# Performance work log

Measured on AMD Instinct MI355X. Metric: run time of the kernel, lower is better.

The kernel has to match this reference:

```python
import jax, jax.numpy as jnp
import numpy as np


def _conv1x1(x, W, b):
    # x: [b,c,h,w], W: [out,in], b: [out]
    return jnp.einsum('oi,bihw->bohw', W, x) + b[None, :, None, None]


def setup_inputs() -> dict:
    key = jax.random.key(0)
    ks = jax.random.split(key, 8)
    B, C, H, W = 4, 256, 64, 64
    s = 1.0 / np.sqrt(C)
    return {
        'x1': jax.random.normal(ks[0], (B, C, H, W), jnp.float32),
        'x2': jax.random.normal(ks[1], (B, C, H, W), jnp.float32),
        'Wq': jax.random.normal(ks[2], (C, C), jnp.float32) * s,
        'bq': jax.random.normal(ks[3], (C,), jnp.float32) * 0.01,
        'Wk': jax.random.normal(ks[4], (C, C), jnp.float32) * s,
        'bk': jax.random.normal(ks[5], (C,), jnp.float32) * 0.01,
        'Wv': jax.random.normal(ks[6], (C, C), jnp.float32) * s,
        'bv': jax.random.normal(ks[7], (C,), jnp.float32) * 0.01,
    }


def reference(x1, x2, Wq, bq, Wk, bk, Wv, bv):
    b, c, h, w = x1.shape
    n = h * w
    q = _conv1x1(x1, Wq, bq).reshape(b, c, n)   # [b,c,n]
    k = _conv1x1(x2, Wk, bk).reshape(b, c, n)   # [b,c,n]
    v = _conv1x1(x2, Wv, bv).reshape(b, c, n)   # [b,c,n]
    # scores[b,i,j] = sum_c q[b,c,i] * k[b,c,j]; softmax over j (last dim)
    scores = jnp.einsum('bci,bcj->bij', q, k)
    attn = jax.nn.softmax(scores, axis=-1)      # [b,n,n]
    # out[b,c,i] = sum_j v[b,c,j] * attn[b,i,j]  (v @ attn^T)
    out = jnp.einsum('bcj,bij->bci', v, attn)
    return out.reshape(b, c, h, w)
```

## Files before the change

### kernel.cpp

```cpp
#include <hip/hip_runtime.h>

#define BATCH 4
#define CDIM 256
#define NDIM 4096
#define SPLITS 4
#define KSPLIT (NDIM / SPLITS)
#define JT 32
#define NTILES (KSPLIT / JT)

typedef unsigned short u16;
typedef unsigned int u32;
typedef _Float16 f16;
typedef __attribute__((ext_vector_type(8))) _Float16 half8;
typedef __attribute__((ext_vector_type(4))) float floatx4;

__device__ __forceinline__ void load_lds_128(const void* g, void* l) {
  __builtin_amdgcn_global_load_lds(
      (const __attribute__((address_space(1))) u32*)g,
      (__attribute__((address_space(3))) u32*)l, 16, 0, 0);
}

__global__ __launch_bounds__(256) void prep_w_k(
    const float* __restrict__ wq, const float* __restrict__ wk,
    const float* __restrict__ wv, f16* __restrict__ whq,
    f16* __restrict__ whk, f16* __restrict__ whv) {
  const int gid = blockIdx.x * 256 + threadIdx.x;
  const int a = gid >> 13;
  const int r = gid & 8191;
  const float* src = (a == 0) ? wq : ((a == 1) ? wk : wv);
  f16* dst = (a == 0) ? whq : ((a == 1) ? whk : whv);
  float4 v0 = *(const float4*)(src + r * 8);
  float4 v1 = *(const float4*)(src + r * 8 + 4);
  half8 h;
  h[0] = (f16)v0.x; h[1] = (f16)v0.y; h[2] = (f16)v0.z; h[3] = (f16)v0.w;
  h[4] = (f16)v1.x; h[5] = (f16)v1.y; h[6] = (f16)v1.z; h[7] = (f16)v1.w;
  *(half8*)(dst + r * 8) = h;
}

__global__ __launch_bounds__(512, 2) void proj_fused_k(
    const float* __restrict__ x1, const float* __restrict__ x2,
    const f16* __restrict__ whq, const float* __restrict__ bq,
    const f16* __restrict__ whk, const float* __restrict__ bk,
    const f16* __restrict__ whv, const float* __restrict__ bv,
    f16* __restrict__ qt, f16* __restrict__ kt, f16* __restrict__ vsp) {
  __shared__ __align__(16) u16 xtt[128 * 264];
  const int j0 = blockIdx.x * 128;
  const int b = blockIdx.y;
  const int z = blockIdx.z;
  const float* xs = ((z == 0) ? x1 : x2) + (size_t)b * CDIM * NDIM;
  const int t = threadIdx.x;
  const int wave = t >> 6, lane = t & 63, l16 = lane & 15, grp = lane >> 4;

#pragma unroll
  for (int it = 0; it < 16; ++it) {
    const int task = wave + it * 8;
    const int c4 = task >> 1;
    const int n = (task & 1) * 64 + lane;
    const float* gp = xs + (size_t)(c4 * 4) * NDIM + j0 + n;
    float v0 = gp[0];
    float v1 = gp[NDIM];
    float v2 = gp[2 * NDIM];
    float v3 = gp[3 * NDIM];
    union { f16 h[4]; uint2 u; } pk;
    pk.h[0] = (f16)v0; pk.h[1] = (f16)v1; pk.h[2] = (f16)v2; pk.h[3] = (f16)v3;
    *(uint2*)&xtt[n * 264 + c4 * 4] = pk.u;
  }
  __syncthreads();
  const f16* xth = (const f16*)xtt;

  {
    const f16* w = (z == 0) ? whq : whk;
    const float* bias = (z == 0) ? bq : bk;
    f16* outp = ((z == 0) ? qt : kt) + (size_t)b * NDIM * CDIM;
    const int jb0 = (wave & 3) * 32;
    const int cw = (wave >> 2) * 128;
    floatx4 acc[2][8];
#pragma unroll
    for (int mb = 0; mb < 2; ++mb)
#pragma unroll
      for (int nb = 0; nb < 8; ++nb) acc[mb][nb] = (floatx4){0.f, 0.f, 0.f, 0.f};
#pragma unroll
    for (int ks = 0; ks < 8; ++ks) {
      half8 a[2];
#pragma unroll
      for (int mb = 0; mb < 2; ++mb) {
        const int n = jb0 + mb * 16 + l16;
        a[mb] = *(const half8*)&xth[n * 264 + ks * 32 + grp * 8];
      }
      __builtin_amdgcn_s_setprio(1);
#pragma unroll
      for (int nb = 0; nb < 8; ++nb) {
        half8 bb = *(const half8*)(w + (size_t)(cw + nb * 16 + l16) * CDIM + ks * 32 + grp * 8);
        acc[0][nb] = __builtin_amdgcn_mfma_f32_16x16x32_f16(a[0], bb, acc[0][nb], 0, 0, 0);
        acc[1][nb] = __builtin_amdgcn_mfma_f32_16x16x32_f16(a[1], bb, acc[1][nb], 0, 0, 0);
      }
      __builtin_amdgcn_s_setprio(0);
    }
#pragma unroll
    for (int nb = 0; nb < 8; ++nb) {
      const int c = cw + nb * 16 + l16;
      const float bvv = bias[c];
#pragma unroll
      for (int mb = 0; mb < 2; ++mb) {
        const int jbase = j0 + jb0 + mb * 16 + grp * 4;
#pragma unroll
        for (int r = 0; r < 4; ++r)
          outp[(size_t)(jbase + r) * CDIM + c] = (f16)(acc[mb][nb][r] + bvv);
      }
    }
  }

  if (z == 1) {
    f16* outp = vsp + (size_t)b * CDIM * NDIM;
    const int cw = (wave & 1) * 128;
    const int jw = (wave >> 1) * 32;
    floatx4 acc[8][2];
#pragma unroll
    for (int mb = 0; mb < 8; ++mb)
#pragma unroll
      for (int nb = 0; nb < 2; ++nb) acc[mb][nb] = (floatx4){0.f, 0.f, 0.f, 0.f};
#pragma unroll
    for (int ks = 0; ks < 8; ++ks) {
      half8 a[8];
#pragma unroll
      for (int mb = 0; mb < 8; ++mb)
        a[mb] = *(const half8*)(whv + (size_t)(cw + mb * 16 + l16) * CDIM + ks * 32 + grp * 8);
#pragma unroll
      for (int nb = 0; nb < 2; ++nb) {
        const int n = jw + nb * 16 + l16;
        half8 bv8 = *(const half8*)&xth[n * 264 + ks * 32 + grp * 8];
        __builtin_amdgcn_s_setprio(1);
#pragma unroll
        for (int mb = 0; mb < 8; ++mb)
          acc[mb][nb] = __builtin_amdgcn_mfma_f32_16x16x32_f16(a[mb], bv8, acc[mb][nb], 0, 0, 0);
        __builtin_amdgcn_s_setprio(0);
      }
    }
#pragma unroll
    for (int mb = 0; mb < 8; ++mb)
#pragma unroll
      for (int r = 0; r < 4; ++r) {
        const int c = cw + mb * 16 + grp * 4 + r;
        const float bvv = bv[c];
#pragma unroll
        for (int nb = 0; nb < 2; ++nb) {
          const int j = j0 + jw + nb * 16 + l16;
          outp[(size_t)c * NDIM + j] = (f16)(acc[mb][nb][r] + bvv);
        }
      }
  }
}

__global__ __launch_bounds__(512, 4) void flash_k(
    const f16* __restrict__ qt, const f16* __restrict__ kt,
    const f16* __restrict__ vs, f16* __restrict__ pO,
    float* __restrict__ pm, float* __restrict__ pl) {
  __shared__ __align__(16) u16 smem[32768 + 5120];
  const int bx = blockIdx.x;
  const int c16 = bx & 15;
  const int b = c16 >> 2, s = c16 & 3;
  const int i0 = (bx >> 4) * 128;
  const int jwin = s * KSPLIT;
  const f16* Q = qt + (size_t)b * NDIM * CDIM;
  const f16* K = kt + (size_t)b * NDIM * CDIM;
  const f16* V = vs + (size_t)b * CDIM * NDIM;
  const int tid = threadIdx.x;
  const int wave = tid >> 6, lane = tid & 63, l16 = lane & 15, grp = lane >> 4;
  f16* Pw = (f16*)(smem + 32768) + wave * (16 * 40);

  half8 qf[8];
#pragma unroll
  for (int ks = 0; ks < 8; ++ks)
    qf[ks] = *(const half8*)(Q + (size_t)(i0 + wave * 16 + l16) * CDIM + ks * 32 + grp * 8);

  floatx4 O[16];
#pragma unroll
  for (int cb = 0; cb < 16; ++cb) O[cb] = (floatx4){0.f, 0.f, 0.f, 0.f};
  float m_ = -1e30f;
  float lsum = 0.f;

  const int kr2 = lane >> 5, kp = lane & 31;
  const int vrow = lane >> 2, vp = lane & 3;

#define STAGE(J0, BUF)                                                         \
  {                                                                            \
    u16* sK = smem + (BUF) * 16384;                                            \
    u16* sV = sK + 8192;                                                       \
    _Pragma("unroll") for (int it = 0; it < 2; ++it) {                         \
      const int row = wave * 4 + it * 2 + kr2;                                 \
      const int g = kp ^ (row & 7);                                            \
      load_lds_128(K + (size_t)((J0) + row) * CDIM + g * 8,                    \
                   &sK[(wave * 4 + it * 2) * 256]);                            \
    }                                                                          \
    _Pragma("unroll") for (int it = 0; it < 2; ++it) {                         \
      const int c = wave * 32 + it * 16 + vrow;                                \
      const int g = vp ^ ((c >> 2) & 3);                                       \
      load_lds_128(V + (size_t)c * NDIM + (J0) + g * 8,                        \
                   &sV[(wave * 32 + it * 16) * 32]);                           \
    }                                                                          \
  }

  STAGE(jwin, 0)

  for (int tt = 0; tt < NTILES; ++tt) {
    __syncthreads();
    if (tt + 1 < NTILES) STAGE(jwin + (tt + 1) * JT, (tt + 1) & 1)
    u16* bK = smem + (tt & 1) * 16384;
    u16* bV = bK + 8192;

    floatx4 S[2];
#pragma unroll
    for (int jb = 0; jb < 2; ++jb) S[jb] = (floatx4){0.f, 0.f, 0.f, 0.f};
    __builtin_amdgcn_s_setprio(1);
#pragma unroll
    for (int ks = 0; ks < 8; ++ks) {
      const int chunk = ks * 4 + grp;
#pragma unroll
      for (int jb = 0; jb < 2; ++jb) {
        const int row = jb * 16 + l16;
        half8 kf = *(const half8*)&bK[row * 256 + ((chunk ^ (row & 7)) << 3)];
        S[jb] = __builtin_amdgcn_mfma_f32_16x16x32_f16(qf[ks], kf, S[jb], 0, 0, 0);
      }
    }
    __builtin_amdgcn_s_setprio(0);

#pragma unroll
    for (int jb = 0; jb < 2; ++jb)
#pragma unroll
      for (int r = 0; r < 4; ++r)
        Pw[(grp * 4 + r) * 40 + jb * 16 + l16] = (f16)S[jb][r];
    half8 rawh = *(const half8*)&Pw[l16 * 40 + grp * 8];
    float u[8];
#pragma unroll
    for (int j = 0; j < 8; ++j) u[j] = (float)rawh[j];
    float mx = fmaxf(fmaxf(fmaxf(u[0], u[1]), fmaxf(u[2], u[3])),
                     fmaxf(fmaxf(u[4], u[5]), fmaxf(u[6], u[7])));
    mx = fmaxf(mx, __shfl_xor(mx, 16, 64));
    mx = fmaxf(mx, __shfl_xor(mx, 32, 64));
    const float mnew = fmaxf(m_, mx);
    const float alpha = __expf(m_ - mnew);
    m_ = mnew;
    float pe[8];
#pragma unroll
    for (int j = 0; j < 8; ++j) pe[j] = __expf(u[j] - mnew);
    const float ps = ((pe[0] + pe[1]) + (pe[2] + pe[3])) +
                     ((pe[4] + pe[5]) + (pe[6] + pe[7]));
    lsum = lsum * alpha + ps;
    half8 pa;
#pragma unroll
    for (int j = 0; j < 8; ++j) pa[j] = (f16)pe[j];

    if (__any(alpha < 1.f)) {
#pragma unroll
      for (int cb = 0; cb < 16; ++cb) O[cb] *= alpha;
    }

    __builtin_amdgcn_s_setprio(1);
#pragma unroll
    for (int cb = 0; cb < 16; ++cb) {
      const int c = cb * 16 + l16;
      half8 vf = *(const half8*)&bV[c * 32 + ((grp ^ ((c >> 2) & 3)) << 3)];
      O[cb] = __builtin_amdgcn_mfma_f32_16x16x32_f16(vf, pa, O[cb], 0, 0, 0);
    }
    __builtin_amdgcn_s_setprio(0);
  }

  lsum += __shfl_xor(lsum, 16, 64);
  lsum += __shfl_xor(lsum, 32, 64);
  if (grp == 0) {
    const int base = (b * SPLITS + s) * NDIM + i0;
    const int i = wave * 16 + l16;
    pm[base + i] = m_;
    pl[base + i] = lsum;
  }

  const size_t pbase = (size_t)(b * SPLITS + s) * CDIM * NDIM;
  const int i = i0 + wave * 16 + l16;
#pragma unroll
  for (int cb = 0; cb < 16; ++cb) {
    const int c = cb * 16 + grp * 4;
#pragma unroll
    for (int r = 0; r < 4; ++r)
      pO[pbase + (size_t)(c + r) * NDIM + i] = (f16)O[cb][r];
  }
}

__global__ __launch_bounds__(256) void combine_k(
    const f16* __restrict__ pO, const float* __restrict__ pm,
    const float* __restrict__ pl, float* __restrict__ out) {
  __shared__ float su[SPLITS][64];
  const int b = blockIdx.x >> 6;
  const int i0 = (blockIdx.x & 63) * 64;
  const int t = threadIdx.x;
  if (t < 64) {
    const int i = i0 + t;
    float mv[SPLITS], w[SPLITS];
    float M = -3e38f;
#pragma unroll
    for (int s = 0; s < SPLITS; ++s) {
      mv[s] = pm[(b * SPLITS + s) * NDIM + i];
      M = fmaxf(M, mv[s]);
    }
    float L = 0.f;
#pragma unroll
    for (int s = 0; s < SPLITS; ++s) {
      w[s] = __expf(mv[s] - M);
      L += pl[(b * SPLITS + s) * NDIM + i] * w[s];
    }
    const float invL = 1.0f / L;
#pragma unroll
    for (int s = 0; s < SPLITS; ++s) su[s][t] = w[s] * invL;
  }
  __syncthreads();
#pragma unroll
  for (int it = 0; it < 8; ++it) {
    const int task = t + it * 256;
    const int c = task >> 3, p = (task & 7) * 8;
    float acc[8] = {0.f, 0.f, 0.f, 0.f, 0.f, 0.f, 0.f, 0.f};
#pragma unroll
    for (int s = 0; s < SPLITS; ++s) {
      const f16* src = pO + ((size_t)(b * SPLITS + s) * CDIM + c) * NDIM + i0 + p;
      half8 h = *(const half8*)src;
#pragma unroll
      for (int j = 0; j < 8; ++j) acc[j] += su[s][p + j] * (float)h[j];
    }
    float* dst = out + ((size_t)b * CDIM + c) * NDIM + i0 + p;
    float4 lo = {acc[0], acc[1], acc[2], acc[3]};
    float4 hi = {acc[4], acc[5], acc[6], acc[7]};
    *(float4*)dst = lo;
    *(float4*)(dst + 4) = hi;
  }
}

extern "C" void kernel_launch(void* const* d_in, const int* in_sizes, int n_in,
                              void* d_out, int out_size, void* d_ws, size_t ws_size,
                              hipStream_t stream) {
  const float* x1 = (const float*)d_in[0];
  const float* x2 = (const float*)d_in[1];
  const float* Wq = (const float*)d_in[2];
  const float* bq = (const float*)d_in[3];
  const float* Wk = (const float*)d_in[4];
  const float* bk = (const float*)d_in[5];
  const float* Wv = (const float*)d_in[6];
  const float* bv = (const float*)d_in[7];
  float* out = (float*)d_out;
  char* ws = (char*)d_ws;
  f16* qtp = (f16*)(ws + 0);
  f16* ktp = (f16*)(ws + 8388608);
  f16* vsp = (f16*)(ws + 16777216);
  f16* pO = (f16*)(ws + 25165824);
  float* pm = (float*)(ws + 58720256);
  float* pl = (float*)(ws + 58982400);
  f16* whq = (f16*)(ws + 41943040);
  f16* whk = whq + CDIM * CDIM;
  f16* whv = whk + CDIM * CDIM;

  prep_w_k<<<dim3(96), dim3(256), 0, stream>>>(Wq, Wk, Wv, whq, whk, whv);
  proj_fused_k<<<dim3(NDIM / 128, BATCH, 2), dim3(512), 0, stream>>>(
      x1, x2, whq, bq, whk, bk, whv, bv, qtp, ktp, vsp);
  flash_k<<<dim3(512), dim3(512), 0, stream>>>(qtp, ktp, vsp, pO, pm, pl);
  combine_k<<<dim3(256), dim3(256), 0, stream>>>(pO, pm, pl, out);
}
```

Before: 249.3 us.

## Single-buffer flash LDS and add 8-way KV split when workspace allows

The flash kernel drops LDS double buffering, loading each K/V tile into a single buffer with a sync before and after compute. This halves shared memory per block so more blocks can be resident. When the workspace is large enough it also uses 8 KV splits with 1024 blocks instead of 4 splits and 512 blocks, which doubles parallelism but doubles the partial-output traffic in the combine step. Without double buffering, global loads no longer overlap with compute inside a block and must be hidden by other resident blocks.

Result: slower. 297.5 us (+19.3%).

```diff
diff --git a/kernel.cpp b/kernel.cpp
--- a/kernel.cpp
+++ b/kernel.cpp
@@ -3,10 +3,7 @@
 #define BATCH 4
 #define CDIM 256
 #define NDIM 4096
-#define SPLITS 4
-#define KSPLIT (NDIM / SPLITS)
 #define JT 32
-#define NTILES (KSPLIT / JT)
 
 typedef unsigned short u16;
 typedef unsigned int u32;
@@ -151,22 +148,25 @@
   }
 }
 
+template <int SPL>
 __global__ __launch_bounds__(512, 4) void flash_k(
     const f16* __restrict__ qt, const f16* __restrict__ kt,
     const f16* __restrict__ vs, f16* __restrict__ pO,
     float* __restrict__ pm, float* __restrict__ pl) {
-  __shared__ __align__(16) u16 smem[32768 + 5120];
+  constexpr int KSP = NDIM / SPL;
+  constexpr int NT = KSP / JT;
+  __shared__ __align__(16) u16 smem[16384 + 5120];
   const int bx = blockIdx.x;
-  const int c16 = bx & 15;
-  const int b = c16 >> 2, s = c16 & 3;
-  const int i0 = (bx >> 4) * 128;
-  const int jwin = s * KSPLIT;
+  const int cc = bx & (BATCH * SPL - 1);
+  const int b = cc / SPL, s = cc % SPL;
+  const int i0 = (bx / (BATCH * SPL)) * 128;
+  const int jwin = s * KSP;
   const f16* Q = qt + (size_t)b * NDIM * CDIM;
   const f16* K = kt + (size_t)b * NDIM * CDIM;
   const f16* V = vs + (size_t)b * CDIM * NDIM;
   const int tid = threadIdx.x;
   const int wave = tid >> 6, lane = tid & 63, l16 = lane & 15, grp = lane >> 4;
-  f16* Pw = (f16*)(smem + 32768) + wave * (16 * 40);
+  f16* Pw = (f16*)(smem + 16384) + wave * (16 * 40);
 
   half8 qf[8];
 #pragma unroll
@@ -182,10 +182,10 @@
   const int kr2 = lane >> 5, kp = lane & 31;
   const int vrow = lane >> 2, vp = lane & 3;
 
-#define STAGE(J0, BUF)                                                         \
+#define STAGE(J0)                                                              \
   {                                                                            \
-    u16* sK = smem + (BUF) * 16384;                                            \
-    u16* sV = sK + 8192;                                                       \
+    u16* sK = smem;                                                            \
+    u16* sV = smem + 8192;                                                     \
     _Pragma("unroll") for (int it = 0; it < 2; ++it) {                         \
       const int row = wave * 4 + it * 2 + kr2;                                 \
       const int g = kp ^ (row & 7);                                            \
@@ -200,13 +200,11 @@
     }                                                                          \
   }
 
-  STAGE(jwin, 0)
-
-  for (int tt = 0; tt < NTILES; ++tt) {
+  for (int tt = 0; tt < NT; ++tt) {
+    STAGE(jwin + tt * JT)
     __syncthreads();
-    if (tt + 1 < NTILES) STAGE(jwin + (tt + 1) * JT, (tt + 1) & 1)
-    u16* bK = smem + (tt & 1) * 16384;
-    u16* bV = bK + 8192;
+    u16* bK = smem;
+    u16* bV = smem + 8192;
 
     floatx4 S[2];
 #pragma unroll
@@ -263,18 +261,19 @@
       O[cb] = __builtin_amdgcn_mfma_f32_16x16x32_f16(vf, pa, O[cb], 0, 0, 0);
     }
     __builtin_amdgcn_s_setprio(0);
+    __syncthreads();
   }
 
   lsum += __shfl_xor(lsum, 16, 64);
   lsum += __shfl_xor(lsum, 32, 64);
   if (grp == 0) {
-    const int base = (b * SPLITS + s) * NDIM + i0;
+    const int base = (b * SPL + s) * NDIM + i0;
     const int i = wave * 16 + l16;
     pm[base + i] = m_;
     pl[base + i] = lsum;
   }
 
-  const size_t pbase = (size_t)(b * SPLITS + s) * CDIM * NDIM;
+  const size_t pbase = (size_t)(b * SPL + s) * CDIM * NDIM;
   const int i = i0 + wave * 16 + l16;
 #pragma unroll
   for (int cb = 0; cb < 16; ++cb) {
@@ -285,31 +284,32 @@
   }
 }
 
+template <int SPL>
 __global__ __launch_bounds__(256) void combine_k(
     const f16* __restrict__ pO, const float* __restrict__ pm,
     const float* __restrict__ pl, float* __restrict__ out) {
-  __shared__ float su[SPLITS][64];
+  __shared__ float su[SPL][64];
   const int b = blockIdx.x >> 6;
   const int i0 = (blockIdx.x & 63) * 64;
   const int t = threadIdx.x;
   if (t < 64) {
     const int i = i0 + t;
-    float mv[SPLITS], w[SPLITS];
+    float mv[SPL], w[SPL];
     float M = -3e38f;
 #pragma unroll
-    for (int s = 0; s < SPLITS; ++s) {
-      mv[s] = pm[(b * SPLITS + s) * NDIM + i];
+    for (int s = 0; s < SPL; ++s) {
+      mv[s] = pm[(b * SPL + s) * NDIM + i];
       M = fmaxf(M, mv[s]);
     }
     float L = 0.f;
 #pragma unroll
-    for (int s = 0; s < SPLITS; ++s) {
+    for (int s = 0; s < SPL; ++s) {
       w[s] = __expf(mv[s] - M);
-      L += pl[(b * SPLITS + s) * NDIM + i] * w[s];
+      L += pl[(b * SPL + s) * NDIM + i] * w[s];
     }
     const float invL = 1.0f / L;
 #pragma unroll
-    for (int s = 0; s < SPLITS; ++s) su[s][t] = w[s] * invL;
+    for (int s = 0; s < SPL; ++s) su[s][t] = w[s] * invL;
   }
   __syncthreads();
 #pragma unroll
@@ -318,8 +318,8 @@
     const int c = task >> 3, p = (task & 7) * 8;
     float acc[8] = {0.f, 0.f, 0.f, 0.f, 0.f, 0.f, 0.f, 0.f};
 #pragma unroll
-    for (int s = 0; s < SPLITS; ++s) {
-      const f16* src = pO + ((size_t)(b * SPLITS + s) * CDIM + c) * NDIM + i0 + p;
+    for (int s = 0; s < SPL; ++s) {
+      const f16* src = pO + ((size_t)(b * SPL + s) * CDIM + c) * NDIM + i0 + p;
       half8 h = *(const half8*)src;
 #pragma unroll
       for (int j = 0; j < 8; ++j) acc[j] += su[s][p + j] * (float)h[j];
@@ -348,16 +348,35 @@
   f16* qtp = (f16*)(ws + 0);
   f16* ktp = (f16*)(ws + 8388608);
   f16* vsp = (f16*)(ws + 16777216);
-  f16* pO = (f16*)(ws + 25165824);
-  float* pm = (float*)(ws + 58720256);
-  float* pl = (float*)(ws + 58982400);
-  f16* whq = (f16*)(ws + 41943040);
+
+  const bool big = ws_size >= 93716480ull;
+
+  f16* pO;
+  float* pm;
+  float* pl;
+  f16* whq;
+  if (big) {
+    pO = (f16*)(ws + 25165824);
+    pm = (float*)(ws + 92274688);
+    pl = (float*)(ws + 92798976);
+    whq = (f16*)(ws + 93323264);
+  } else {
+    pO = (f16*)(ws + 25165824);
+    pm = (float*)(ws + 58720256);
+    pl = (float*)(ws + 58982400);
+    whq = (f16*)(ws + 41943040);
+  }
   f16* whk = whq + CDIM * CDIM;
   f16* whv = whk + CDIM * CDIM;
 
   prep_w_k<<<dim3(96), dim3(256), 0, stream>>>(Wq, Wk, Wv, whq, whk, whv);
   proj_fused_k<<<dim3(NDIM / 128, BATCH, 2), dim3(512), 0, stream>>>(
       x1, x2, whq, bq, whk, bk, whv, bv, qtp, ktp, vsp);
-  flash_k<<<dim3(512), dim3(512), 0, stream>>>(qtp, ktp, vsp, pO, pm, pl);
-  combine_k<<<dim3(256), dim3(256), 0, stream>>>(pO, pm, pl, out);
-}
+  if (big) {
+    flash_k<8><<<dim3(1024), dim3(512), 0, stream>>>(qtp, ktp, vsp, pO, pm, pl);
+    combine_k<8><<<dim3(256), dim3(256), 0, stream>>>(pO, pm, pl, out);
+  } else {
+    flash_k<4><<<dim3(512), dim3(512), 0, stream>>>(qtp, ktp, vsp, pO, pm, pl);
+    combine_k<4><<<dim3(256), dim3(256), 0, stream>>>(pO, pm, pl, out);
+  }
+}
```
